# Kernel optimization log

Hardware: AMD Instinct MI355X
Metric: run time of the kernel (lower is better)

The kernel has to match this reference:

```python
import jax, jax.numpy as jnp
import numpy as np

B, D, N, K = 4, 256, 4096, 8192


def setup_inputs() -> dict:
    key = jax.random.key(0)
    kx, ke = jax.random.split(key)
    x = jax.random.normal(kx, (B, D, N), dtype=jnp.float32)
    e = jax.random.normal(ke, (K, D), dtype=jnp.float32)
    return {"x": x, "e": e}


def reference(x, e):
    # encode: cdist(x^T [B,N,D], e [K,D]) -> [B,N,K]; argmin over K.
    # sqrt is monotonic, so argmin of squared distance == argmin of cdist.
    xt = jnp.transpose(x, (0, 2, 1))                      # [B,N,D]
    x2 = jnp.sum(xt * xt, axis=-1, keepdims=True)         # [B,N,1]
    e2 = jnp.sum(e * e, axis=-1)                          # [K]
    d2 = x2 - 2.0 * jnp.einsum('bnd,kd->bnk', xt, e) + e2 # [B,N,K]
    codes = jnp.argmin(d2, axis=-1)                       # [B,N]
    # decode: embedding gather then transpose back to [B,D,N]
    quantized = e[codes]                                  # [B,N,D]
    return jnp.transpose(quantized, (0, 2, 1))            # [B,D,N]
```

## Files before the change

### kernel.cpp

```cpp
#include <hip/hip_runtime.h>
#include <stdint.h>

#define B_ 4
#define D_ 256
#define N_ 4096
#define K_ 8192
#define Q_ (B_*N_)

typedef __attribute__((ext_vector_type(8))) short bf16x8;
typedef __attribute__((ext_vector_type(16))) float f32x16;

__device__ __forceinline__ unsigned short f32_to_bf16(float f) {
  unsigned u = __float_as_uint(f);
  unsigned r = 0x7FFFu + ((u >> 16) & 1u);
  return (unsigned short)((u + r) >> 16);
}
__device__ __forceinline__ float bf16_to_f32(unsigned short h) {
  return __uint_as_float(((unsigned)h) << 16);
}

__device__ __forceinline__ void gl_lds16(const void* g, void* l) {
  __builtin_amdgcn_global_load_lds(
      (const __attribute__((address_space(1))) unsigned int*)g,
      (__attribute__((address_space(3))) unsigned int*)l, 16, 0, 0);
}

__global__ void prep_x_kernel(const float* __restrict__ x,
                              unsigned short* __restrict__ xh,
                              unsigned short* __restrict__ xl) {
  __shared__ float tile[32][33];
  int b = blockIdx.z;
  int d0 = blockIdx.y * 32;
  int n0 = blockIdx.x * 32;
  int tx = threadIdx.x, ty = threadIdx.y;
  const float* xp = x + ((size_t)b * D_ + d0) * N_ + n0;
#pragma unroll
  for (int i = 0; i < 4; ++i)
    tile[ty + 8 * i][tx] = xp[(size_t)(ty + 8 * i) * N_ + tx];
  __syncthreads();
#pragma unroll
  for (int i = 0; i < 4; ++i) {
    int nl = ty + 8 * i;
    float v = tile[tx][nl];
    unsigned short h = f32_to_bf16(v);
    unsigned short l = f32_to_bf16(v - bf16_to_f32(h));
    size_t q = (size_t)b * N_ + n0 + nl;
    xh[q * D_ + d0 + tx] = h;
    xl[q * D_ + d0 + tx] = l;
  }
}

__global__ void prep_e_kernel(const float* __restrict__ e,
                              unsigned short* __restrict__ eh,
                              unsigned short* __restrict__ el,
                              float* __restrict__ e2h,
                              unsigned long long* __restrict__ keys) {
  int k = blockIdx.x;
  int d = threadIdx.x;
  if (d < 2) keys[(size_t)k * 2 + d] = ~0ull;
  float v = e[(size_t)k * D_ + d];
  unsigned short h = f32_to_bf16(v);
  unsigned short l = f32_to_bf16(v - bf16_to_f32(h));
  eh[(size_t)k * D_ + d] = h;
  el[(size_t)k * D_ + d] = l;
  float s = v * v;
#pragma unroll
  for (int off = 32; off > 0; off >>= 1) s += __shfl_down(s, off, 64);
  __shared__ float ws4[4];
  if ((threadIdx.x & 63) == 0) ws4[threadIdx.x >> 6] = s;
  __syncthreads();
  if (threadIdx.x == 0) e2h[k] = 0.5f * (ws4[0] + ws4[1] + ws4[2] + ws4[3]);
}

__global__ __launch_bounds__(512, 2) void vq_main_kernel(
    const unsigned short* __restrict__ xh, const unsigned short* __restrict__ xl,
    const unsigned short* __restrict__ eh, const unsigned short* __restrict__ el,
    const float* __restrict__ e2h, unsigned long long* __restrict__ keys) {
  __shared__ __attribute__((aligned(16))) unsigned short Bs[2][2][32 * 256];

  const int tid = threadIdx.x;
  const int w = tid >> 6;
  const int lane = tid & 63;
  const int l = lane & 31;
  const int hi = lane >> 5;

  const int qt = blockIdx.x >> 2;
  const int ks4 = blockIdx.x & 3;
  const int q0 = qt * 256;
  const int kbase = ks4 * 2048;
  const int qw = q0 + w * 32;

  bf16x8 ah[16], al[16];
  {
    const unsigned short* pa = xh + (size_t)(qw + l) * D_ + hi * 8;
    const unsigned short* pb = xl + (size_t)(qw + l) * D_ + hi * 8;
#pragma unroll
    for (int kc16 = 0; kc16 < 16; ++kc16) {
      ah[kc16] = *(const bf16x8*)(pa + kc16 * 16);
      al[kc16] = *(const bf16x8*)(pb + kc16 * 16);
    }
  }

  float rminv[16];
  int rmini[16];
#pragma unroll
  for (int r = 0; r < 16; ++r) { rminv[r] = __builtin_inff(); rmini[r] = 0; }

  auto stage = [&](int ch, int buf) {
    const int kc = kbase + ch * 32;
#pragma unroll
    for (int p = 0; p < 2; ++p) {
      const int c0 = w * 4 + p * 2;
      const int c = c0 + hi;
      const int g = l ^ (c & 31);
      const size_t srcoff = (size_t)(kc + c) * D_ + g * 8;
      gl_lds16(eh + srcoff, &Bs[buf][0][c0 * 256]);
      gl_lds16(el + srcoff, &Bs[buf][1][c0 * 256]);
    }
  };

  stage(0, 0);

#pragma unroll 1
  for (int ch = 0; ch < 64; ++ch) {
    const int buf = ch & 1;
    __syncthreads();
    if (ch + 1 < 64) stage(ch + 1, buf ^ 1);
    const int kc = kbase + ch * 32;
    const float e2v = e2h[kc + l];

    f32x16 acc;
#pragma unroll
    for (int r = 0; r < 16; ++r) acc[r] = 0.f;

#pragma unroll
    for (int ks = 0; ks < 16; ++ks) {
      const int pos = (((ks * 2 + hi) ^ l) * 8);
      bf16x8 bh = *(const bf16x8*)&Bs[buf][0][l * 256 + pos];
      bf16x8 bl = *(const bf16x8*)&Bs[buf][1][l * 256 + pos];
      acc = __builtin_amdgcn_mfma_f32_32x32x16_bf16(ah[ks], bh, acc, 0, 0, 0);
      acc = __builtin_amdgcn_mfma_f32_32x32x16_bf16(ah[ks], bl, acc, 0, 0, 0);
      acc = __builtin_amdgcn_mfma_f32_32x32x16_bf16(al[ks], bh, acc, 0, 0, 0);
    }

    const int kidx = kc + l;
#pragma unroll
    for (int r = 0; r < 16; ++r) {
      float dv = e2v - acc[r];
      bool better = dv < rminv[r];
      rminv[r] = better ? dv : rminv[r];
      rmini[r] = better ? kidx : rmini[r];
    }
  }

#pragma unroll
  for (int r = 0; r < 16; ++r) {
    float bv = rminv[r];
    int bi = rmini[r];
#pragma unroll
    for (int xm = 1; xm <= 16; xm <<= 1) {
      float ov = __shfl_xor(bv, xm, 64);
      int oi = __shfl_xor(bi, xm, 64);
      if (ov < bv || (ov == bv && oi < bi)) { bv = ov; bi = oi; }
    }
    if (l == 0) {
      const int m = (r & 3) + 8 * (r >> 2) + 4 * hi;
      const int qq = qw + m;
      unsigned su = __float_as_uint(bv);
      su ^= (unsigned)(((int)su >> 31) | 0x80000000u);
      unsigned long long key = ((unsigned long long)su << 32) | (unsigned)bi;
      atomicMin(keys + qq, key);
    }
  }
}

__global__ void decode_kernel(const unsigned long long* __restrict__ keys,
                              const float* __restrict__ e,
                              float* __restrict__ out) {
  size_t gid = (size_t)blockIdx.x * 256 + threadIdx.x;
  int n = (int)(gid % N_);
  int rest = (int)(gid / N_);
  int d = rest % D_;
  int b = rest / D_;
  unsigned idx = (unsigned)(keys[(size_t)b * N_ + n] & 0xFFFFFFFFull);
  out[gid] = e[(size_t)idx * D_ + d];
}

extern "C" void kernel_launch(void* const* d_in, const int* in_sizes, int n_in,
                              void* d_out, int out_size, void* d_ws, size_t ws_size,
                              hipStream_t stream) {
  const float* x = (const float*)d_in[0];
  const float* e = (const float*)d_in[1];
  float* out = (float*)d_out;

  char* wksp = (char*)d_ws;
  unsigned short* xh = (unsigned short*)wksp;
  unsigned short* xl = xh + (size_t)Q_ * D_;
  unsigned short* eh = xl + (size_t)Q_ * D_;
  unsigned short* el = eh + (size_t)K_ * D_;
  float* e2h = (float*)(el + (size_t)K_ * D_);
  unsigned long long* keys = (unsigned long long*)(e2h + K_);

  prep_x_kernel<<<dim3(N_ / 32, D_ / 32, B_), dim3(32, 8), 0, stream>>>(x, xh, xl);
  prep_e_kernel<<<K_, 256, 0, stream>>>(e, eh, el, e2h, keys);
  vq_main_kernel<<<256, 512, 0, stream>>>(xh, xl, eh, el, e2h, keys);
  decode_kernel<<<(Q_ * D_) / 256, 256, 0, stream>>>(keys, e, out);
}
```

Baseline: 260.6 us.

## Split codebook across more blocks and vectorize transpose and decode kernels

New measurement: 571.3 us. 119% more time.

```diff
diff --git a/kernel.cpp b/kernel.cpp
--- a/kernel.cpp
+++ b/kernel.cpp
@@ -8,6 +8,7 @@
 #define Q_ (B_*N_)
 
 typedef __attribute__((ext_vector_type(8))) short bf16x8;
+typedef __attribute__((ext_vector_type(8))) unsigned short u16x8;
 typedef __attribute__((ext_vector_type(16))) float f32x16;
 
 __device__ __forceinline__ unsigned short f32_to_bf16(float f) {
@@ -28,25 +29,41 @@
 __global__ void prep_x_kernel(const float* __restrict__ x,
                               unsigned short* __restrict__ xh,
                               unsigned short* __restrict__ xl) {
-  __shared__ float tile[32][33];
+  __shared__ float tile[64][65];
   int b = blockIdx.z;
-  int d0 = blockIdx.y * 32;
-  int n0 = blockIdx.x * 32;
-  int tx = threadIdx.x, ty = threadIdx.y;
+  int d0 = blockIdx.y * 64;
+  int n0 = blockIdx.x * 64;
+  int tid = threadIdx.x;
+
+  int rr = tid >> 4;
+  int rc = (tid & 15) * 4;
   const float* xp = x + ((size_t)b * D_ + d0) * N_ + n0;
 #pragma unroll
-  for (int i = 0; i < 4; ++i)
-    tile[ty + 8 * i][tx] = xp[(size_t)(ty + 8 * i) * N_ + tx];
+  for (int p = 0; p < 4; ++p) {
+    float4 v = *(const float4*)(xp + (size_t)(rr + 16 * p) * N_ + rc);
+    tile[rr + 16 * p][rc + 0] = v.x;
+    tile[rr + 16 * p][rc + 1] = v.y;
+    tile[rr + 16 * p][rc + 2] = v.z;
+    tile[rr + 16 * p][rc + 3] = v.w;
+  }
   __syncthreads();
-#pragma unroll
-  for (int i = 0; i < 4; ++i) {
-    int nl = ty + 8 * i;
-    float v = tile[tx][nl];
-    unsigned short h = f32_to_bf16(v);
-    unsigned short l = f32_to_bf16(v - bf16_to_f32(h));
-    size_t q = (size_t)b * N_ + n0 + nl;
-    xh[q * D_ + d0 + tx] = h;
-    xl[q * D_ + d0 + tx] = l;
+
+  int nr = tid >> 3;
+  int dc = tid & 7;
+#pragma unroll
+  for (int p = 0; p < 2; ++p) {
+    int nn = nr + 32 * p;
+    u16x8 h8, l8;
+#pragma unroll
+    for (int j = 0; j < 8; ++j) {
+      float v = tile[dc * 8 + j][nn];
+      unsigned short h = f32_to_bf16(v);
+      h8[j] = h;
+      l8[j] = f32_to_bf16(v - bf16_to_f32(h));
+    }
+    size_t q = (size_t)b * N_ + n0 + nn;
+    *(u16x8*)(xh + q * D_ + d0 + dc * 8) = h8;
+    *(u16x8*)(xl + q * D_ + d0 + dc * 8) = l8;
   }
 }
 
@@ -72,7 +89,7 @@
   if (threadIdx.x == 0) e2h[k] = 0.5f * (ws4[0] + ws4[1] + ws4[2] + ws4[3]);
 }
 
-__global__ __launch_bounds__(512, 2) void vq_main_kernel(
+__global__ __launch_bounds__(512, 4) void vq_main_kernel(
     const unsigned short* __restrict__ xh, const unsigned short* __restrict__ xl,
     const unsigned short* __restrict__ eh, const unsigned short* __restrict__ el,
     const float* __restrict__ e2h, unsigned long long* __restrict__ keys) {
@@ -84,10 +101,10 @@
   const int l = lane & 31;
   const int hi = lane >> 5;
 
-  const int qt = blockIdx.x >> 2;
-  const int ks4 = blockIdx.x & 3;
+  const int qt = blockIdx.x >> 3;
+  const int ks8 = blockIdx.x & 7;
   const int q0 = qt * 256;
-  const int kbase = ks4 * 2048;
+  const int kbase = ks8 * 1024;
   const int qw = q0 + w * 32;
 
   bf16x8 ah[16], al[16];
@@ -122,10 +139,10 @@
   stage(0, 0);
 
 #pragma unroll 1
-  for (int ch = 0; ch < 64; ++ch) {
+  for (int ch = 0; ch < 32; ++ch) {
     const int buf = ch & 1;
     __syncthreads();
-    if (ch + 1 < 64) stage(ch + 1, buf ^ 1);
+    if (ch + 1 < 32) stage(ch + 1, buf ^ 1);
     const int kc = kbase + ch * 32;
     const float e2v = e2h[kc + l];
 
@@ -178,12 +195,18 @@
                               const float* __restrict__ e,
                               float* __restrict__ out) {
   size_t gid = (size_t)blockIdx.x * 256 + threadIdx.x;
-  int n = (int)(gid % N_);
-  int rest = (int)(gid / N_);
+  int nq = (int)(gid % (N_ / 4));
+  int rest = (int)(gid / (N_ / 4));
   int d = rest % D_;
   int b = rest / D_;
-  unsigned idx = (unsigned)(keys[(size_t)b * N_ + n] & 0xFFFFFFFFull);
-  out[gid] = e[(size_t)idx * D_ + d];
+  int n0 = nq * 4;
+  const unsigned long long* kp = keys + (size_t)b * N_ + n0;
+  float4 o;
+  o.x = e[(size_t)(unsigned)(kp[0] & 0xFFFFFFFFull) * D_ + d];
+  o.y = e[(size_t)(unsigned)(kp[1] & 0xFFFFFFFFull) * D_ + d];
+  o.z = e[(size_t)(unsigned)(kp[2] & 0xFFFFFFFFull) * D_ + d];
+  o.w = e[(size_t)(unsigned)(kp[3] & 0xFFFFFFFFull) * D_ + d];
+  *(float4*)(out + ((size_t)b * D_ + d) * N_ + n0) = o;
 }
 
 extern "C" void kernel_launch(void* const* d_in, const int* in_sizes, int n_in,
@@ -201,8 +224,8 @@
   float* e2h = (float*)(el + (size_t)K_ * D_);
   unsigned long long* keys = (unsigned long long*)(e2h + K_);
 
-  prep_x_kernel<<<dim3(N_ / 32, D_ / 32, B_), dim3(32, 8), 0, stream>>>(x, xh, xl);
+  prep_x_kernel<<<dim3(N_ / 64, D_ / 64, B_), 256, 0, stream>>>(x, xh, xl);
   prep_e_kernel<<<K_, 256, 0, stream>>>(e, eh, el, e2h, keys);
-  vq_main_kernel<<<256, 512, 0, stream>>>(xh, xl, eh, el, e2h, keys);
-  decode_kernel<<<(Q_ * D_) / 256, 256, 0, stream>>>(keys, e, out);
-}
+  vq_main_kernel<<<512, 512, 0, stream>>>(xh, xl, eh, el, e2h, keys);
+  decode_kernel<<<(Q_ * D_) / 1024, 256, 0, stream>>>(keys, e, out);
+}
```
